# Optimization experiments

Measured on AMD Instinct MI355X. Metric: run time of the kernel, lower is better.

The kernel has to match this reference:

```python
import jax, jax.numpy as jnp
import numpy as np

N = 100000   # nodes
E = 1600000  # edges (avg degree 16)
D = 64       # feature dim (in_dim)


def setup_inputs() -> dict:
    key = jax.random.key(0)
    k1, k2, k3, k4, k5 = jax.random.split(key, 5)
    h = jax.random.normal(k1, (N, D), dtype=jnp.float32)
    dnorm = jax.random.uniform(k2, (N,), dtype=jnp.float32)  # deg^-1/2 proxy
    # xavier_normal_(gain=1.414) for Linear(2D, 1): std = gain*sqrt(2/(fan_in+fan_out))
    std = 1.414 * np.sqrt(2.0 / (2 * D + 1))
    gate_w = jax.random.normal(k3, (1, 2 * D), dtype=jnp.float32) * std
    gate_b = jnp.zeros((1,), dtype=jnp.float32)
    src = jax.random.randint(k4, (E,), 0, N, dtype=jnp.int32)
    dst = jax.random.randint(k5, (E,), 0, N, dtype=jnp.int32)
    return {"h": h, "dnorm": dnorm, "gate_w": gate_w, "gate_b": gate_b,
            "src": src, "dst": dst}


def reference(h, dnorm, gate_w, gate_b, src, dst):
    # gate(cat[h_dst, h_src]) == h_dst @ W[:, :D].T + h_src @ W[:, D:].T + b
    w_dst = gate_w[0, :D]  # [D]
    w_src = gate_w[0, D:]  # [D]
    h_src = h[src]                                        # [E, D] gather
    g = jnp.tanh(h[dst] @ w_dst + h_src @ w_src + gate_b[0])  # [E]
    e = g * dnorm[dst] * dnorm[src]                       # [E] (dropout p=0 -> identity)
    # u_mul_e + sum: z[v] = sum_{(u->v)} h[u] * e
    z = jax.ops.segment_sum(h_src * e[:, None], dst, num_segments=N)  # [N, D]
    return z
```

## Files before the change

### kernel.cpp

```cpp
#include <hip/hip_runtime.h>
#include <hip/hip_bf16.h>

#define D 64
#define NB_MAX 512
#define BKT_SHIFT 8
#define BKT_NODES 256
#define DSPLIT_T 512
#define DSPLIT_E 4096
#define CAP 5120

__device__ __forceinline__ unsigned short f2bf(float x) {
    unsigned u = __float_as_uint(x);
    unsigned r = 0x7fffu + ((u >> 16) & 1u);
    return (unsigned short)((u + r) >> 16);
}

template<bool MAKE_BF16>
__global__ void fal_precompute(const float* __restrict__ h,
                               const float* __restrict__ dnorm,
                               const float* __restrict__ gate_w,
                               const float* __restrict__ gate_b,
                               float2* __restrict__ sd,
                               float2* __restrict__ ss,
                               unsigned short* __restrict__ hb,
                               int N) {
    int tid  = threadIdx.x;
    int lane = tid & 63;
    int wave = tid >> 6;
    int grp  = lane >> 4;
    int gl   = lane & 15;

    int node = blockIdx.x * 16 + wave * 4 + grp;
    int nc   = node < N ? node : N - 1;

    const float4* h4 = (const float4*)h;
    const float4* w4 = (const float4*)gate_w;

    float4 hv  = h4[nc * 16 + gl];
    float4 wd  = w4[gl];
    float4 wsr = w4[16 + gl];

    if (MAKE_BF16 && node < N) {
        ushort4 p = make_ushort4(f2bf(hv.x), f2bf(hv.y), f2bf(hv.z), f2bf(hv.w));
        *(ushort4*)&hb[(size_t)node * D + gl * 4] = p;
    }

    float a = hv.x * wd.x + hv.y * wd.y + hv.z * wd.z + hv.w * wd.w;
    float b = hv.x * wsr.x + hv.y * wsr.y + hv.z * wsr.z + hv.w * wsr.w;

    for (int off = 1; off < 16; off <<= 1) {
        a += __shfl_xor(a, off, 64);
        b += __shfl_xor(b, off, 64);
    }

    if (gl == 0 && node < N) {
        float dn = dnorm[node];
        sd[node] = make_float2(a + gate_b[0], dn);
        ss[node] = make_float2(b, dn);
    }
}

__global__ __launch_bounds__(DSPLIT_T) void fal_multisplit(
        const int* __restrict__ src,
        const int* __restrict__ dst,
        int* __restrict__ bcursor,
        unsigned* __restrict__ pk_bin,
        int E, int nb) {
    __shared__ int lcount[NB_MAX];
    __shared__ int lscan[NB_MAX];
    __shared__ int gofs[NB_MAX];
    __shared__ int wsum[8];
    __shared__ unsigned s_pk[DSPLIT_E];
    __shared__ int s_gpos[DSPLIT_E];

    int tid  = threadIdx.x;
    int lane = tid & 63;
    int w    = tid >> 6;
    lcount[tid] = 0;
    __syncthreads();

    int E4 = E >> 2;
    int e4base = blockIdx.x * (DSPLIT_E / 4);

    int srcs[8], dsts[8], lr[8];
    #pragma unroll
    for (int g = 0; g < 2; ++g) {
        int i4 = e4base + g * DSPLIT_T + tid;
        if (i4 < E4) {
            int4 s4 = ((const int4*)src)[i4];
            int4 d4 = ((const int4*)dst)[i4];
            int sa[4] = {s4.x, s4.y, s4.z, s4.w};
            int da[4] = {d4.x, d4.y, d4.z, d4.w};
            #pragma unroll
            for (int j = 0; j < 4; ++j) {
                int k = g * 4 + j;
                srcs[k] = sa[j];
                dsts[k] = da[j];
                lr[k]   = atomicAdd(&lcount[da[j] >> BKT_SHIFT], 1);
            }
        }
    }
    __syncthreads();

    int v = lcount[tid];
    for (int off = 1; off < 64; off <<= 1) {
        int t = __shfl_up(v, off, 64);
        if (lane >= off) v += t;
    }
    if (lane == 63) wsum[w] = v;
    __syncthreads();
    if (tid < 8) {
        int s = wsum[tid];
        for (int off = 1; off < 8; off <<= 1) {
            int t = __shfl_up(s, off, 64);
            if (tid >= off) s += t;
        }
        wsum[tid] = s;
    }
    __syncthreads();
    lscan[tid] = v + (w ? wsum[w - 1] : 0);

    if (tid < nb) {
        int c = lcount[tid];
        int rel = c ? atomicAdd(&bcursor[tid], c) : 0;
        gofs[tid] = tid * CAP + rel;
    }
    __syncthreads();

    #pragma unroll
    for (int g = 0; g < 2; ++g) {
        int i4 = e4base + g * DSPLIT_T + tid;
        if (i4 < E4) {
            #pragma unroll
            for (int j = 0; j < 4; ++j) {
                int k = g * 4 + j;
                int b = dsts[k] >> BKT_SHIFT;
                int lpos = (lscan[b] - lcount[b]) + lr[k];
                unsigned dl = (unsigned)(dsts[k] & (BKT_NODES - 1));
                s_pk[lpos] = (dl << 20) | (unsigned)srcs[k];
                int gp = gofs[b] + lr[k];
                s_gpos[lpos] = (gp < (b + 1) * CAP) ? gp : -1;
            }
        }
    }
    __syncthreads();

    int total = lscan[NB_MAX - 1];
    for (int t = tid; t < total; t += DSPLIT_T) {
        int g = s_gpos[t];
        if (g >= 0) pk_bin[g] = s_pk[t];
    }
}

template<bool BF16>
__global__ __launch_bounds__(1024) void fal_bucket_process(
        const float* __restrict__ h,
        const unsigned short* __restrict__ hb,
        const float2* __restrict__ sd,
        const float2* __restrict__ ss,
        const int* __restrict__ bcursor,
        const unsigned* __restrict__ pk_bin,
        float* __restrict__ z, int N) {
    __shared__ unsigned s_pk[CAP];
    __shared__ unsigned s_srt[CAP];
    __shared__ float    s_esc[CAP];
    __shared__ float2   sdl[BKT_NODES];
    __shared__ int nhist[BKT_NODES];
    __shared__ int nbase[BKT_NODES];
    __shared__ int ncur[BKT_NODES];
    __shared__ int wsum16[16];

    int b    = blockIdx.x;
    int tid  = threadIdx.x;
    int lane = tid & 63;
    int w    = tid >> 6;

    if (tid < BKT_NODES) {
        nhist[tid] = 0;
        int node = b * BKT_NODES + tid;
        sdl[tid] = (node < N) ? sd[node] : make_float2(0.f, 0.f);
    }
    __syncthreads();

    int cnt = min(bcursor[b], CAP);
    const unsigned* bin = pk_bin + (size_t)b * CAP;

    for (int t = tid; t < cnt; t += 1024) {
        unsigned pk = bin[t];
        s_pk[t] = pk;
        atomicAdd(&nhist[pk >> 20], 1);
    }
    __syncthreads();

    int myh = (tid < BKT_NODES) ? nhist[tid] : 0;
    int v = myh;
    for (int off = 1; off < 64; off <<= 1) {
        int t = __shfl_up(v, off, 64);
        if (lane >= off) v += t;
    }
    if (lane == 63) wsum16[w] = v;
    __syncthreads();
    if (tid < 16) {
        int s2 = wsum16[tid];
        for (int off = 1; off < 16; off <<= 1) {
            int t = __shfl_up(s2, off, 64);
            if (tid >= off) s2 += t;
        }
        wsum16[tid] = s2;
    }
    __syncthreads();
    if (tid < BKT_NODES) {
        int incl = v + (w ? wsum16[w - 1] : 0);
        nbase[tid] = incl - myh;
        ncur[tid]  = 0;
    }
    __syncthreads();

    for (int t = tid; t < cnt; t += 1024) {
        unsigned pk = s_pk[t];
        int dl = (int)(pk >> 20);
        int sn = (int)(pk & 0xFFFFFu);
        int r  = atomicAdd(&ncur[dl], 1);
        float2 sv = ss[sn];
        float2 dv = sdl[dl];
        float esc = tanhf(dv.x + sv.x) * dv.y * sv.y;
        int p = nbase[dl] + r;
        s_srt[p] = pk;
        s_esc[p] = esc;
    }
    __syncthreads();

    int o    = lane >> 3;
    int sdim = lane & 7;

    for (int ni = 0; ni < BKT_NODES / 16; ++ni) {
        int dl   = w * 16 + ni;
        int seg0 = nbase[dl];
        int dg   = nhist[dl];

        float acc[8];
        #pragma unroll
        for (int i = 0; i < 8; ++i) acc[i] = 0.0f;

        for (int k0 = 0; k0 < dg; k0 += 64) {
            int c = min(64, dg - k0);

            int   s_l = 0;
            float e_l = 0.0f;
            if (lane < c) {
                unsigned pk = s_srt[seg0 + k0 + lane];
                s_l = (int)(pk & 0xFFFFFu);
                e_l = s_esc[seg0 + k0 + lane];
            }

            for (int j = 0; j < c; j += 8) {
                int e  = j + o;
                int   sj = __shfl(s_l, e, 64);
                float ej = __shfl(e_l, e, 64);
                if (BF16) {
                    uint4 hv = *(const uint4*)&hb[(size_t)sj * D + sdim * 8];
                    acc[0] = fmaf(__uint_as_float(hv.x << 16),         ej, acc[0]);
                    acc[1] = fmaf(__uint_as_float(hv.x & 0xffff0000u), ej, acc[1]);
                    acc[2] = fmaf(__uint_as_float(hv.y << 16),         ej, acc[2]);
                    acc[3] = fmaf(__uint_as_float(hv.y & 0xffff0000u), ej, acc[3]);
                    acc[4] = fmaf(__uint_as_float(hv.z << 16),         ej, acc[4]);
                    acc[5] = fmaf(__uint_as_float(hv.z & 0xffff0000u), ej, acc[5]);
                    acc[6] = fmaf(__uint_as_float(hv.w << 16),         ej, acc[6]);
                    acc[7] = fmaf(__uint_as_float(hv.w & 0xffff0000u), ej, acc[7]);
                } else {
                    const float4* hp = (const float4*)&h[(size_t)sj * D + sdim * 8];
                    float4 h0 = hp[0], h1 = hp[1];
                    acc[0] = fmaf(h0.x, ej, acc[0]);
                    acc[1] = fmaf(h0.y, ej, acc[1]);
                    acc[2] = fmaf(h0.z, ej, acc[2]);
                    acc[3] = fmaf(h0.w, ej, acc[3]);
                    acc[4] = fmaf(h1.x, ej, acc[4]);
                    acc[5] = fmaf(h1.y, ej, acc[5]);
                    acc[6] = fmaf(h1.z, ej, acc[6]);
                    acc[7] = fmaf(h1.w, ej, acc[7]);
                }
            }
        }

        #pragma unroll
        for (int m = 8; m < 64; m <<= 1) {
            #pragma unroll
            for (int i = 0; i < 8; ++i)
                acc[i] += __shfl_xor(acc[i], m, 64);
        }

        if (o == 0) {
            int node = b * BKT_NODES + dl;
            if (node < N) {
                float4* zp = (float4*)&z[(size_t)node * D + sdim * 8];
                zp[0] = make_float4(acc[0], acc[1], acc[2], acc[3]);
                zp[1] = make_float4(acc[4], acc[5], acc[6], acc[7]);
            }
        }
    }
}

extern "C" void kernel_launch(void* const* d_in, const int* in_sizes, int n_in,
                              void* d_out, int out_size, void* d_ws, size_t ws_size,
                              hipStream_t stream) {
    const float* h      = (const float*)d_in[0];
    const float* dnorm  = (const float*)d_in[1];
    const float* gate_w = (const float*)d_in[2];
    const float* gate_b = (const float*)d_in[3];
    const int*   src    = (const int*)d_in[4];
    const int*   dst    = (const int*)d_in[5];
    float*       z      = (float*)d_out;

    int N  = in_sizes[1];
    int E  = in_sizes[4];
    int nb = (N + BKT_NODES - 1) >> BKT_SHIFT;

    char* ws0 = (char*)d_ws;
    size_t off = 0;
    auto alloc = [&](size_t bytes) {
        char* p = ws0 + off;
        off += (bytes + 15) & ~(size_t)15;
        return p;
    };
    float2*   sd      = (float2*)alloc((size_t)N * sizeof(float2));
    float2*   ss      = (float2*)alloc((size_t)N * sizeof(float2));
    int*      bcursor = (int*)alloc((size_t)nb * sizeof(int));
    unsigned* pk_bin  = (unsigned*)alloc((size_t)nb * CAP * sizeof(unsigned));
    unsigned short* hb = (unsigned short*)(ws0 + off);
    size_t need_with_hb = off + (size_t)N * D * sizeof(unsigned short);
    bool use_bf16 = (ws_size >= need_with_hb);

    hipMemsetAsync(bcursor, 0, (size_t)nb * sizeof(int), stream);

    if (use_bf16)
        fal_precompute<true><<<(N + 15) / 16, 256, 0, stream>>>(
            h, dnorm, gate_w, gate_b, sd, ss, hb, N);
    else
        fal_precompute<false><<<(N + 15) / 16, 256, 0, stream>>>(
            h, dnorm, gate_w, gate_b, sd, ss, hb, N);

    fal_multisplit<<<(E + DSPLIT_E - 1) / DSPLIT_E, DSPLIT_T, 0, stream>>>(
        src, dst, bcursor, pk_bin, E, nb);

    if (use_bf16)
        fal_bucket_process<true><<<nb, 1024, 0, stream>>>(
            h, hb, sd, ss, bcursor, pk_bin, z, N);
    else
        fal_bucket_process<false><<<nb, 1024, 0, stream>>>(
            h, hb, sd, ss, bcursor, pk_bin, z, N);
}
```

Baseline: 174.0 us.

## Halve bucket size and assign each dst node to an 8-lane group

Buckets shrink from 256 to 128 nodes (782 buckets, CAP 2560), so the multisplit kernel grows to 1024 threads handling one int4 per thread. The bucket-process kernel drops to 512 threads. Each 8-lane group now owns one destination node and walks its edges serially, two at a time, instead of a whole wavefront cooperating per node with shuffles and a cross-lane reduction. This removes shuffle and reduction overhead and the idle lanes on low-degree nodes, but it creates load imbalance across lanes when degrees vary and gives fewer concurrent gathers per node.

```diff
diff --git a/kernel.cpp b/kernel.cpp
--- a/kernel.cpp
+++ b/kernel.cpp
@@ -2,12 +2,12 @@
 #include <hip/hip_bf16.h>
 
 #define D 64
-#define NB_MAX 512
-#define BKT_SHIFT 8
-#define BKT_NODES 256
-#define DSPLIT_T 512
+#define BKT_SHIFT 7
+#define BKT_NODES 128
+#define NB_CNT 1024
+#define DSPLIT_T 1024
 #define DSPLIT_E 4096
-#define CAP 5120
+#define CAP 2560
 
 __device__ __forceinline__ unsigned short f2bf(float x) {
     unsigned u = __float_as_uint(x);
@@ -66,10 +66,10 @@
         int* __restrict__ bcursor,
         unsigned* __restrict__ pk_bin,
         int E, int nb) {
-    __shared__ int lcount[NB_MAX];
-    __shared__ int lscan[NB_MAX];
-    __shared__ int gofs[NB_MAX];
-    __shared__ int wsum[8];
+    __shared__ int lcount[NB_CNT];
+    __shared__ int lscan[NB_CNT];
+    __shared__ int gofs[NB_CNT];
+    __shared__ int wsum16[16];
     __shared__ unsigned s_pk[DSPLIT_E];
     __shared__ int s_gpos[DSPLIT_E];
 
@@ -80,25 +80,18 @@
     __syncthreads();
 
     int E4 = E >> 2;
-    int e4base = blockIdx.x * (DSPLIT_E / 4);
-
-    int srcs[8], dsts[8], lr[8];
-    #pragma unroll
-    for (int g = 0; g < 2; ++g) {
-        int i4 = e4base + g * DSPLIT_T + tid;
-        if (i4 < E4) {
-            int4 s4 = ((const int4*)src)[i4];
-            int4 d4 = ((const int4*)dst)[i4];
-            int sa[4] = {s4.x, s4.y, s4.z, s4.w};
-            int da[4] = {d4.x, d4.y, d4.z, d4.w};
-            #pragma unroll
-            for (int j = 0; j < 4; ++j) {
-                int k = g * 4 + j;
-                srcs[k] = sa[j];
-                dsts[k] = da[j];
-                lr[k]   = atomicAdd(&lcount[da[j] >> BKT_SHIFT], 1);
-            }
-        }
+    int i4 = blockIdx.x * DSPLIT_T + tid;
+
+    int srcs[4], dsts[4], lr[4];
+    bool act = (i4 < E4);
+    if (act) {
+        int4 s4 = ((const int4*)src)[i4];
+        int4 d4 = ((const int4*)dst)[i4];
+        srcs[0] = s4.x; srcs[1] = s4.y; srcs[2] = s4.z; srcs[3] = s4.w;
+        dsts[0] = d4.x; dsts[1] = d4.y; dsts[2] = d4.z; dsts[3] = d4.w;
+        #pragma unroll
+        for (int j = 0; j < 4; ++j)
+            lr[j] = atomicAdd(&lcount[dsts[j] >> BKT_SHIFT], 1);
     }
     __syncthreads();
 
@@ -107,18 +100,18 @@
         int t = __shfl_up(v, off, 64);
         if (lane >= off) v += t;
     }
-    if (lane == 63) wsum[w] = v;
-    __syncthreads();
-    if (tid < 8) {
-        int s = wsum[tid];
-        for (int off = 1; off < 8; off <<= 1) {
+    if (lane == 63) wsum16[w] = v;
+    __syncthreads();
+    if (tid < 16) {
+        int s = wsum16[tid];
+        for (int off = 1; off < 16; off <<= 1) {
             int t = __shfl_up(s, off, 64);
             if (tid >= off) s += t;
         }
-        wsum[tid] = s;
-    }
-    __syncthreads();
-    lscan[tid] = v + (w ? wsum[w - 1] : 0);
+        wsum16[tid] = s;
+    }
+    __syncthreads();
+    lscan[tid] = v + (w ? wsum16[w - 1] : 0);
 
     if (tid < nb) {
         int c = lcount[tid];
@@ -127,25 +120,20 @@
     }
     __syncthreads();
 
-    #pragma unroll
-    for (int g = 0; g < 2; ++g) {
-        int i4 = e4base + g * DSPLIT_T + tid;
-        if (i4 < E4) {
-            #pragma unroll
-            for (int j = 0; j < 4; ++j) {
-                int k = g * 4 + j;
-                int b = dsts[k] >> BKT_SHIFT;
-                int lpos = (lscan[b] - lcount[b]) + lr[k];
-                unsigned dl = (unsigned)(dsts[k] & (BKT_NODES - 1));
-                s_pk[lpos] = (dl << 20) | (unsigned)srcs[k];
-                int gp = gofs[b] + lr[k];
-                s_gpos[lpos] = (gp < (b + 1) * CAP) ? gp : -1;
-            }
-        }
-    }
-    __syncthreads();
-
-    int total = lscan[NB_MAX - 1];
+    if (act) {
+        #pragma unroll
+        for (int j = 0; j < 4; ++j) {
+            int b = dsts[j] >> BKT_SHIFT;
+            int lpos = (lscan[b] - lcount[b]) + lr[j];
+            unsigned dl = (unsigned)(dsts[j] & (BKT_NODES - 1));
+            s_pk[lpos] = (dl << 20) | (unsigned)srcs[j];
+            int gp = gofs[b] + lr[j];
+            s_gpos[lpos] = (gp < (b + 1) * CAP) ? gp : -1;
+        }
+    }
+    __syncthreads();
+
+    int total = lscan[NB_CNT - 1];
     for (int t = tid; t < total; t += DSPLIT_T) {
         int g = s_gpos[t];
         if (g >= 0) pk_bin[g] = s_pk[t];
@@ -153,7 +141,7 @@
 }
 
 template<bool BF16>
-__global__ __launch_bounds__(1024) void fal_bucket_process(
+__global__ __launch_bounds__(512) void fal_bucket_process(
         const float* __restrict__ h,
         const unsigned short* __restrict__ hb,
         const float2* __restrict__ sd,
@@ -168,7 +156,7 @@
     __shared__ int nhist[BKT_NODES];
     __shared__ int nbase[BKT_NODES];
     __shared__ int ncur[BKT_NODES];
-    __shared__ int wsum16[16];
+    __shared__ int wsum8[8];
 
     int b    = blockIdx.x;
     int tid  = threadIdx.x;
@@ -185,7 +173,7 @@
     int cnt = min(bcursor[b], CAP);
     const unsigned* bin = pk_bin + (size_t)b * CAP;
 
-    for (int t = tid; t < cnt; t += 1024) {
+    for (int t = tid; t < cnt; t += 512) {
         unsigned pk = bin[t];
         s_pk[t] = pk;
         atomicAdd(&nhist[pk >> 20], 1);
@@ -198,25 +186,25 @@
         int t = __shfl_up(v, off, 64);
         if (lane >= off) v += t;
     }
-    if (lane == 63) wsum16[w] = v;
-    __syncthreads();
-    if (tid < 16) {
-        int s2 = wsum16[tid];
-        for (int off = 1; off < 16; off <<= 1) {
+    if (lane == 63) wsum8[w] = v;
+    __syncthreads();
+    if (tid < 8) {
+        int s2 = wsum8[tid];
+        for (int off = 1; off < 8; off <<= 1) {
             int t = __shfl_up(s2, off, 64);
             if (tid >= off) s2 += t;
         }
-        wsum16[tid] = s2;
+        wsum8[tid] = s2;
     }
     __syncthreads();
     if (tid < BKT_NODES) {
-        int incl = v + (w ? wsum16[w - 1] : 0);
+        int incl = v + (w ? wsum8[w - 1] : 0);
         nbase[tid] = incl - myh;
         ncur[tid]  = 0;
     }
     __syncthreads();
 
-    for (int t = tid; t < cnt; t += 1024) {
+    for (int t = tid; t < cnt; t += 512) {
         unsigned pk = s_pk[t];
         int dl = (int)(pk >> 20);
         int sn = (int)(pk & 0xFFFFFu);
@@ -230,11 +218,12 @@
     }
     __syncthreads();
 
-    int o    = lane >> 3;
-    int sdim = lane & 7;
-
-    for (int ni = 0; ni < BKT_NODES / 16; ++ni) {
-        int dl   = w * 16 + ni;
+    int oct  = tid >> 3;
+    int sdim = tid & 7;
+
+    #pragma unroll
+    for (int ni = 0; ni < BKT_NODES / 64; ++ni) {
+        int dl   = oct + ni * 64;
         int seg0 = nbase[dl];
         int dg   = nhist[dl];
 
@@ -242,60 +231,76 @@
         #pragma unroll
         for (int i = 0; i < 8; ++i) acc[i] = 0.0f;
 
-        for (int k0 = 0; k0 < dg; k0 += 64) {
-            int c = min(64, dg - k0);
-
-            int   s_l = 0;
-            float e_l = 0.0f;
-            if (lane < c) {
-                unsigned pk = s_srt[seg0 + k0 + lane];
-                s_l = (int)(pk & 0xFFFFFu);
-                e_l = s_esc[seg0 + k0 + lane];
+        int k = 0;
+        for (; k + 2 <= dg; k += 2) {
+            unsigned p0 = s_srt[seg0 + k];
+            unsigned p1 = s_srt[seg0 + k + 1];
+            float    e0 = s_esc[seg0 + k];
+            float    e1 = s_esc[seg0 + k + 1];
+            int s0 = (int)(p0 & 0xFFFFFu);
+            int s1 = (int)(p1 & 0xFFFFFu);
+            if (BF16) {
+                uint4 a0 = *(const uint4*)&hb[(size_t)s0 * D + sdim * 8];
+                uint4 a1 = *(const uint4*)&hb[(size_t)s1 * D + sdim * 8];
+                acc[0] = fmaf(__uint_as_float(a0.x << 16),         e0, acc[0]);
+                acc[1] = fmaf(__uint_as_float(a0.x & 0xffff0000u), e0, acc[1]);
+                acc[2] = fmaf(__uint_as_float(a0.y << 16),         e0, acc[2]);
+                acc[3] = fmaf(__uint_as_float(a0.y & 0xffff0000u), e0, acc[3]);
+                acc[4] = fmaf(__uint_as_float(a0.z << 16),         e0, acc[4]);
+                acc[5] = fmaf(__uint_as_float(a0.z & 0xffff0000u), e0, acc[5]);
+                acc[6] = fmaf(__uint_as_float(a0.w << 16),         e0, acc[6]);
+                acc[7] = fmaf(__uint_as_float(a0.w & 0xffff0000u), e0, acc[7]);
+                acc[0] = fmaf(__uint_as_float(a1.x << 16),         e1, acc[0]);
+                acc[1] = fmaf(__uint_as_float(a1.x & 0xffff0000u), e1, acc[1]);
+                acc[2] = fmaf(__uint_as_float(a1.y << 16),         e1, acc[2]);
+                acc[3] = fmaf(__uint_as_float(a1.y & 0xffff0000u), e1, acc[3]);
+                acc[4] = fmaf(__uint_as_float(a1.z << 16),         e1, acc[4]);
+                acc[5] = fmaf(__uint_as_float(a1.z & 0xffff0000u), e1, acc[5]);
+                acc[6] = fmaf(__uint_as_float(a1.w << 16),         e1, acc[6]);
+                acc[7] = fmaf(__uint_as_float(a1.w & 0xffff0000u), e1, acc[7]);
+            } else {
+                const float4* hp0 = (const float4*)&h[(size_t)s0 * D + sdim * 8];
+                const float4* hp1 = (const float4*)&h[(size_t)s1 * D + sdim * 8];
+                float4 q0 = hp0[0], q1 = hp0[1], q2 = hp1[0], q3 = hp1[1];
+                acc[0] = fmaf(q0.x, e0, acc[0]); acc[1] = fmaf(q0.y, e0, acc[1]);
+                acc[2] = fmaf(q0.z, e0, acc[2]); acc[3] = fmaf(q0.w, e0, acc[3]);
+                acc[4] = fmaf(q1.x, e0, acc[4]); acc[5] = fmaf(q1.y, e0, acc[5]);
+                acc[6] = fmaf(q1.z, e0, acc[6]); acc[7] = fmaf(q1.w, e0, acc[7]);
+                acc[0] = fmaf(q2.x, e1, acc[0]); acc[1] = fmaf(q2.y, e1, acc[1]);
+                acc[2] = fmaf(q2.z, e1, acc[2]); acc[3] = fmaf(q2.w, e1, acc[3]);
+                acc[4] = fmaf(q3.x, e1, acc[4]); acc[5] = fmaf(q3.y, e1, acc[5]);
+                acc[6] = fmaf(q3.z, e1, acc[6]); acc[7] = fmaf(q3.w, e1, acc[7]);
             }
-
-            for (int j = 0; j < c; j += 8) {
-                int e  = j + o;
-                int   sj = __shfl(s_l, e, 64);
-                float ej = __shfl(e_l, e, 64);
-                if (BF16) {
-                    uint4 hv = *(const uint4*)&hb[(size_t)sj * D + sdim * 8];
-                    acc[0] = fmaf(__uint_as_float(hv.x << 16),         ej, acc[0]);
-                    acc[1] = fmaf(__uint_as_float(hv.x & 0xffff0000u), ej, acc[1]);
-                    acc[2] = fmaf(__uint_as_float(hv.y << 16),         ej, acc[2]);
-                    acc[3] = fmaf(__uint_as_float(hv.y & 0xffff0000u), ej, acc[3]);
-                    acc[4] = fmaf(__uint_as_float(hv.z << 16),         ej, acc[4]);
-                    acc[5] = fmaf(__uint_as_float(hv.z & 0xffff0000u), ej, acc[5]);
-                    acc[6] = fmaf(__uint_as_float(hv.w << 16),         ej, acc[6]);
-                    acc[7] = fmaf(__uint_as_float(hv.w & 0xffff0000u), ej, acc[7]);
-                } else {
-                    const float4* hp = (const float4*)&h[(size_t)sj * D + sdim * 8];
-                    float4 h0 = hp[0], h1 = hp[1];
-                    acc[0] = fmaf(h0.x, ej, acc[0]);
-                    acc[1] = fmaf(h0.y, ej, acc[1]);
-                    acc[2] = fmaf(h0.z, ej, acc[2]);
-                    acc[3] = fmaf(h0.w, ej, acc[3]);
-                    acc[4] = fmaf(h1.x, ej, acc[4]);
-                    acc[5] = fmaf(h1.y, ej, acc[5]);
-                    acc[6] = fmaf(h1.z, ej, acc[6]);
-                    acc[7] = fmaf(h1.w, ej, acc[7]);
-                }
+        }
+        if (k < dg) {
+            unsigned p0 = s_srt[seg0 + k];
+            float    e0 = s_esc[seg0 + k];
+            int s0 = (int)(p0 & 0xFFFFFu);
+            if (BF16) {
+                uint4 a0 = *(const uint4*)&hb[(size_t)s0 * D + sdim * 8];
+                acc[0] = fmaf(__uint_as_float(a0.x << 16),         e0, acc[0]);
+                acc[1] = fmaf(__uint_as_float(a0.x & 0xffff0000u), e0, acc[1]);
+                acc[2] = fmaf(__uint_as_float(a0.y << 16),         e0, acc[2]);
+                acc[3] = fmaf(__uint_as_float(a0.y & 0xffff0000u), e0, acc[3]);
+                acc[4] = fmaf(__uint_as_float(a0.z << 16),         e0, acc[4]);
+                acc[5] = fmaf(__uint_as_float(a0.z & 0xffff0000u), e0, acc[5]);
+                acc[6] = fmaf(__uint_as_float(a0.w << 16),         e0, acc[6]);
+                acc[7] = fmaf(__uint_as_float(a0.w & 0xffff0000u), e0, acc[7]);
+            } else {
+                const float4* hp0 = (const float4*)&h[(size_t)s0 * D + sdim * 8];
+                float4 q0 = hp0[0], q1 = hp0[1];
+                acc[0] = fmaf(q0.x, e0, acc[0]); acc[1] = fmaf(q0.y, e0, acc[1]);
+                acc[2] = fmaf(q0.z, e0, acc[2]); acc[3] = fmaf(q0.w, e0, acc[3]);
+                acc[4] = fmaf(q1.x, e0, acc[4]); acc[5] = fmaf(q1.y, e0, acc[5]);
+                acc[6] = fmaf(q1.z, e0, acc[6]); acc[7] = fmaf(q1.w, e0, acc[7]);
             }
         }
 
-        #pragma unroll
-        for (int m = 8; m < 64; m <<= 1) {
-            #pragma unroll
-            for (int i = 0; i < 8; ++i)
-                acc[i] += __shfl_xor(acc[i], m, 64);
-        }
-
-        if (o == 0) {
-            int node = b * BKT_NODES + dl;
-            if (node < N) {
-                float4* zp = (float4*)&z[(size_t)node * D + sdim * 8];
-                zp[0] = make_float4(acc[0], acc[1], acc[2], acc[3]);
-                zp[1] = make_float4(acc[4], acc[5], acc[6], acc[7]);
-            }
+        int node = b * BKT_NODES + dl;
+        if (node < N) {
+            float4* zp = (float4*)&z[(size_t)node * D + sdim * 8];
+            zp[0] = make_float4(acc[0], acc[1], acc[2], acc[3]);
+            zp[1] = make_float4(acc[4], acc[5], acc[6], acc[7]);
         }
     }
 }
@@ -343,9 +348,9 @@
         src, dst, bcursor, pk_bin, E, nb);
 
     if (use_bf16)
-        fal_bucket_process<true><<<nb, 1024, 0, stream>>>(
+        fal_bucket_process<true><<<nb, 512, 0, stream>>>(
             h, hb, sd, ss, bcursor, pk_bin, z, N);
     else
-        fal_bucket_process<false><<<nb, 1024, 0, stream>>>(
+        fal_bucket_process<false><<<nb, 512, 0, stream>>>(
             h, hb, sd, ss, bcursor, pk_bin, z, N);
 }
```

Result: faster. 169.7 us (-2.5%).
